# Optimization experiments

Measured on AMD Instinct MI355X. Metric: run time of the kernel, lower is better.

The kernel has to match this reference:

```python
import jax, jax.numpy as jnp
import numpy as np

LAYER_NUM = 2
HEAD_NUM = 2
LN_EPS = 1e-3  # Keras LayerNormalization default epsilon


def setup_inputs() -> dict:
    key = jax.random.key(0)
    ks = jax.random.split(key, 8)
    B, F, E = 16384, 40, 64
    s = 1.0 / np.sqrt(E)
    return {
        "x": jax.random.normal(ks[0], (B, F, E), jnp.float32),
        "Wq": jax.random.normal(ks[1], (E, E), jnp.float32) * s,
        "bq": jnp.zeros((E,), jnp.float32),
        "Wk": jax.random.normal(ks[2], (E, E), jnp.float32) * s,
        "bk": jnp.zeros((E,), jnp.float32),
        "Wv": jax.random.normal(ks[3], (E, E), jnp.float32) * s,
        "bv": jnp.zeros((E,), jnp.float32),
        "Wr": jax.random.normal(ks[4], (E, E), jnp.float32) * s,
        "br": jnp.zeros((E,), jnp.float32),
        "gamma": jnp.ones((E,), jnp.float32),
        "beta": jnp.zeros((E,), jnp.float32),
    }


def _split_heads(t, H):
    # [B, F, E] -> [B, H, F, E//H]; equivalent to tf split(axis=2)+concat(axis=0)
    B, F, E = t.shape
    return t.reshape(B, F, H, E // H).transpose(0, 2, 1, 3)


def _merge_heads(t):
    # [B, H, F, Dh] -> [B, F, E]
    B, H, F, Dh = t.shape
    return t.transpose(0, 2, 1, 3).reshape(B, F, H * Dh)


def reference(x, Wq, bq, Wk, bk, Wv, bv, Wr, br, gamma, beta):
    H = HEAD_NUM
    out = x
    for _ in range(LAYER_NUM):  # same (shared) weights every iteration, as in Keras build()
        q = jax.nn.relu(out @ Wq + bq)
        k = jax.nn.relu(out @ Wk + bk)
        v = jax.nn.relu(out @ Wv + bv)
        res = jax.nn.relu(out @ Wr + br)
        qh = _split_heads(q, H)  # [B,H,F,Dh]
        kh = _split_heads(k, H)
        vh = _split_heads(v, H)
        Dh = qh.shape[-1]
        w = jnp.einsum("bhfd,bhgd->bhfg", qh, kh) / jnp.sqrt(jnp.float32(Dh))
        w = jax.nn.softmax(w, axis=-1)
        # dropout_rate=0.0 -> no dropout branch in the original module
        o = jnp.einsum("bhfg,bhgd->bhfd", w, vh)
        out = _merge_heads(o) + res
        out = jax.nn.relu(out)
        mu = jnp.mean(out, axis=-1, keepdims=True)
        var = jnp.mean(jnp.square(out - mu), axis=-1, keepdims=True)
        out = (out - mu) * jax.lax.rsqrt(var + LN_EPS) * gamma + beta
    return out
```

## Files before the change

kernel.cpp:

```cpp
#include <hip/hip_runtime.h>
#include <math.h>

#define TF 40
#define FP 48
#define TE 64
#define RS 72
#define NTH 256
#define CURSZ (FP * RS)

typedef __attribute__((ext_vector_type(8))) short bf16x8;
typedef __attribute__((ext_vector_type(4))) float f32x4;
typedef unsigned int uint;
typedef unsigned short ushort;

#define MFMA(a, b, c) __builtin_amdgcn_mfma_f32_16x16x32_bf16(a, b, c, 0, 0, 0)

__device__ __forceinline__ ushort f2bf(float x) {
    union { float f; uint u; } a; a.f = x;
    uint r = a.u + 0x7FFFu + ((a.u >> 16) & 1u);
    return (ushort)(r >> 16);
}
__device__ __forceinline__ float bf2f(ushort h) {
    union { uint u; float f; } a; a.u = ((uint)h) << 16;
    return a.f;
}

__global__ void prep_wfrags(const float* __restrict__ Wq, const float* __restrict__ Wk,
                            const float* __restrict__ Wv, const float* __restrict__ Wr,
                            ushort* __restrict__ wsf) {
    int idx = blockIdx.x * blockDim.x + threadIdx.x;
    int j    = idx & 7;
    int lane = (idx >> 3) & 63;
    int et   = (idx >> 9) & 3;
    int k2   = (idx >> 11) & 1;
    int mat  = (idx >> 12) & 3;
    const float* W = (mat == 0) ? Wq : (mat == 1) ? Wk : (mat == 2) ? Wv : Wr;
    int k = k2 * 32 + (lane >> 4) * 8 + j;
    int e = et * 16 + (lane & 15);
    wsf[idx] = f2bf(W[k * TE + e]);
}

__global__ __launch_bounds__(NTH)
void autoint_mfma(const float* __restrict__ x,
                  const float* __restrict__ bq, const float* __restrict__ bk,
                  const float* __restrict__ bv, const float* __restrict__ br,
                  const float* __restrict__ gamma, const float* __restrict__ beta,
                  const ushort* __restrict__ wsf,
                  float* __restrict__ out) {
    __shared__ ushort sCur[2][CURSZ];
    __shared__ ushort sQ[CURSZ];
    __shared__ ushort sK[CURSZ];
    __shared__ ushort sVT[TE * RS];
    __shared__ float  sRed[2][4][FP];

    const int t  = threadIdx.x;
    const int w  = t >> 6;
    const int l  = t & 63;
    const int r0 = l & 15;
    const int kg = l >> 4;
    const int ec = 16 * w + r0;
    const size_t base = (size_t)blockIdx.x * (TF * TE);

    const float bQ = bq[ec], bK = bk[ec], bV = bv[ec], bR = br[ec];
    const float gV = gamma[ec], btV = beta[ec];

    const bf16x8* wsv = (const bf16x8*)wsf;
    const bf16x8 wq0 = wsv[((0*2+0)*4 + w)*64 + l], wq1 = wsv[((0*2+1)*4 + w)*64 + l];
    const bf16x8 wk0 = wsv[((1*2+0)*4 + w)*64 + l], wk1 = wsv[((1*2+1)*4 + w)*64 + l];
    const bf16x8 wv0 = wsv[((2*2+0)*4 + w)*64 + l], wv1 = wsv[((2*2+1)*4 + w)*64 + l];
    const bf16x8 wr0 = wsv[((3*2+0)*4 + w)*64 + l], wr1 = wsv[((3*2+1)*4 + w)*64 + l];

    {
        const float4* xb4 = (const float4*)(x + base);
        for (int i = t; i < TF * TE / 4; i += NTH) {
            float4 xv = xb4[i];
            int f = i >> 4, c = (i & 15) << 2;
            ushort h0 = f2bf(xv.x), h1 = f2bf(xv.y), h2 = f2bf(xv.z), h3 = f2bf(xv.w);
            uint2 ph; ph.x = h0 | ((uint)h1 << 16); ph.y = h2 | ((uint)h3 << 16);
            *(uint2*)&sCur[0][f * RS + c] = ph;
            ushort l0 = f2bf(xv.x - bf2f(h0)), l1 = f2bf(xv.y - bf2f(h1));
            ushort l2 = f2bf(xv.z - bf2f(h2)), l3 = f2bf(xv.w - bf2f(h3));
            uint2 pl; pl.x = l0 | ((uint)l1 << 16); pl.y = l2 | ((uint)l3 << 16);
            *(uint2*)&sCur[1][f * RS + c] = pl;
        }
        for (int i = t; i < 576; i += NTH) {
            int part = i / 288, rem = i - part * 288;
            int row = 40 + rem / 36, c = rem % 36;
            ((uint*)&sCur[part][0])[row * 36 + c] = 0u;
        }
        for (int i = t; i < 768; i += NTH) {
            int row = i / 12, c = i % 12;
            ((uint*)&sVT[0])[row * 36 + 24 + c] = 0u;
        }
    }
    __syncthreads();

    for (int lay = 0; lay < 2; ++lay) {
        f32x4 res0, res1, res2;
        #pragma unroll
        for (int ft = 0; ft < 3; ++ft) {
            const int rowb = (ft * 16 + r0) * RS + kg * 8;
            bf16x8 ah0 = *(const bf16x8*)&sCur[0][rowb];
            bf16x8 ah1 = *(const bf16x8*)&sCur[0][rowb + 32];
            bf16x8 al0 = *(const bf16x8*)&sCur[1][rowb];
            bf16x8 al1 = *(const bf16x8*)&sCur[1][rowb + 32];
            f32x4 z = {0.f, 0.f, 0.f, 0.f};
            f32x4 aq = z, ak = z, av = z, ar = z;
            aq = MFMA(ah0, wq0, aq); aq = MFMA(ah1, wq1, aq);
            aq = MFMA(al0, wq0, aq); aq = MFMA(al1, wq1, aq);
            ak = MFMA(ah0, wk0, ak); ak = MFMA(ah1, wk1, ak);
            ak = MFMA(al0, wk0, ak); ak = MFMA(al1, wk1, ak);
            av = MFMA(ah0, wv0, av); av = MFMA(ah1, wv1, av);
            av = MFMA(al0, wv0, av); av = MFMA(al1, wv1, av);
            ar = MFMA(ah0, wr0, ar); ar = MFMA(ah1, wr1, ar);
            ar = MFMA(al0, wr0, ar); ar = MFMA(al1, wr1, ar);
            ushort pv[4];
            f32x4 rr;
            #pragma unroll
            for (int r = 0; r < 4; ++r) {
                const int fr = ft * 16 + 4 * kg + r;
                sQ[fr * RS + ec] = f2bf(fmaxf(aq[r] + bQ, 0.f));
                sK[fr * RS + ec] = f2bf(fmaxf(ak[r] + bK, 0.f));
                pv[r] = f2bf(fmaxf(av[r] + bV, 0.f));
                rr[r] = fmaxf(ar[r] + bR, 0.f);
            }
            uint2 pk; pk.x = pv[0] | ((uint)pv[1] << 16); pk.y = pv[2] | ((uint)pv[3] << 16);
            *(uint2*)&sVT[ec * RS + ft * 16 + 4 * kg] = pk;
            if (ft == 0) res0 = rr; else if (ft == 1) res1 = rr; else res2 = rr;
        }
        __syncthreads();

        for (int i = t; i < 768; i += NTH) {
            int ph = i / 384, rem = i - ph * 384;
            int row = rem >> 3, c = rem & 7;
            ((uint*)&sCur[ph][0])[row * 36 + 24 + c] = 0u;
        }

        auto p2unit = [&](int u) {
            const int h  = (u >= 3) ? 1 : 0;
            const int ft = u - 3 * h;
            const int co = 32 * h + kg * 8;
            bf16x8 a  = *(const bf16x8*)&sQ[(ft * 16 + r0) * RS + co];
            bf16x8 b0 = *(const bf16x8*)&sK[(r0) * RS + co];
            bf16x8 b1 = *(const bf16x8*)&sK[(16 + r0) * RS + co];
            bf16x8 b2 = *(const bf16x8*)&sK[(32 + r0) * RS + co];
            f32x4 z = {0.f, 0.f, 0.f, 0.f};
            f32x4 c0 = MFMA(a, b0, z);
            f32x4 c1 = MFMA(a, b1, z);
            f32x4 c2 = MFMA(a, b2, z);
            ushort* Ph = &sCur[h][0];
            #pragma unroll
            for (int r = 0; r < 4; ++r) {
                const float SC = 0.17677669529663687f;
                float v0 = c0[r] * SC, v1 = c1[r] * SC;
                float v2 = (r0 < 8) ? c2[r] * SC : -3.0e38f;
                float m = fmaxf(fmaxf(v0, v1), v2);
                m = fmaxf(m, __shfl_xor(m, 1)); m = fmaxf(m, __shfl_xor(m, 2));
                m = fmaxf(m, __shfl_xor(m, 4)); m = fmaxf(m, __shfl_xor(m, 8));
                float p0 = exp2f((v0 - m) * 1.44269504f);
                float p1 = exp2f((v1 - m) * 1.44269504f);
                float p2 = (r0 < 8) ? exp2f((v2 - m) * 1.44269504f) : 0.f;
                float s = p0 + p1 + p2;
                s += __shfl_xor(s, 1); s += __shfl_xor(s, 2);
                s += __shfl_xor(s, 4); s += __shfl_xor(s, 8);
                float inv = 1.0f / s;
                const int fr = ft * 16 + 4 * kg + r;
                Ph[fr * RS +      r0] = f2bf(p0 * inv);
                Ph[fr * RS + 16 + r0] = f2bf(p1 * inv);
                Ph[fr * RS + 32 + r0] = f2bf(p2 * inv);
            }
        };
        p2unit(w);
        if (w < 2) p2unit(w + 4);
        __syncthreads();

        const int h = w >> 1;
        const ushort* Ph = &sCur[h][0];
        bf16x8 vb0 = *(const bf16x8*)&sVT[ec * RS + kg * 8];
        bf16x8 vb1 = *(const bf16x8*)&sVT[ec * RS + 32 + kg * 8];
        float vo0[4], vo1[4], vo2[4];
        #pragma unroll
        for (int ft = 0; ft < 3; ++ft) {
            bf16x8 pa0 = *(const bf16x8*)&Ph[(ft * 16 + r0) * RS + kg * 8];
            bf16x8 pa1 = *(const bf16x8*)&Ph[(ft * 16 + r0) * RS + 32 + kg * 8];
            f32x4 o = (ft == 0) ? res0 : (ft == 1) ? res1 : res2;
            o = MFMA(pa0, vb0, o);
            o = MFMA(pa1, vb1, o);
            #pragma unroll
            for (int r = 0; r < 4; ++r) {
                float v = fmaxf(o[r], 0.f);
                if (ft == 0) vo0[r] = v; else if (ft == 1) vo1[r] = v; else vo2[r] = v;
            }
        }

        #pragma unroll
        for (int ft = 0; ft < 3; ++ft) {
            #pragma unroll
            for (int r = 0; r < 4; ++r) {
                float v = (ft == 0) ? vo0[r] : (ft == 1) ? vo1[r] : vo2[r];
                float a = v, b = v * v;
                a += __shfl_xor(a, 1); b += __shfl_xor(b, 1);
                a += __shfl_xor(a, 2); b += __shfl_xor(b, 2);
                a += __shfl_xor(a, 4); b += __shfl_xor(b, 4);
                a += __shfl_xor(a, 8); b += __shfl_xor(b, 8);
                if (r0 == 0) {
                    const int fr = ft * 16 + 4 * kg + r;
                    sRed[0][w][fr] = a;
                    sRed[1][w][fr] = b;
                }
            }
        }
        __syncthreads();

        #pragma unroll
        for (int ft = 0; ft < 3; ++ft) {
            #pragma unroll
            for (int r = 0; r < 4; ++r) {
                const int fr = ft * 16 + 4 * kg + r;
                float v  = (ft == 0) ? vo0[r] : (ft == 1) ? vo1[r] : vo2[r];
                float s1 = sRed[0][0][fr] + sRed[0][1][fr] + sRed[0][2][fr] + sRed[0][3][fr];
                float s2 = sRed[1][0][fr] + sRed[1][1][fr] + sRed[1][2][fr] + sRed[1][3][fr];
                float mu  = s1 * 0.015625f;
                float var = fmaf(s2, 0.015625f, -mu * mu);
                float yv  = (v - mu) * rsqrtf(var + 1e-3f) * gV + btV;
                if (fr < TF) {
                    if (lay == 0) {
                        ushort hh = f2bf(yv);
                        sCur[0][fr * RS + ec] = hh;
                        sCur[1][fr * RS + ec] = f2bf(yv - bf2f(hh));
                    } else {
                        out[base + fr * TE + ec] = yv;
                    }
                }
            }
        }
        __syncthreads();
    }
}

extern "C" void kernel_launch(void* const* d_in, const int* in_sizes, int n_in,
                              void* d_out, int out_size, void* d_ws, size_t ws_size,
                              hipStream_t stream) {
    const float* x     = (const float*)d_in[0];
    const float* Wq    = (const float*)d_in[1];
    const float* bq    = (const float*)d_in[2];
    const float* Wk    = (const float*)d_in[3];
    const float* bk    = (const float*)d_in[4];
    const float* Wv    = (const float*)d_in[5];
    const float* bv    = (const float*)d_in[6];
    const float* Wr    = (const float*)d_in[7];
    const float* br    = (const float*)d_in[8];
    const float* gamma = (const float*)d_in[9];
    const float* beta  = (const float*)d_in[10];
    float* outp = (float*)d_out;
    ushort* wsf = (ushort*)d_ws;

    prep_wfrags<<<64, 256, 0, stream>>>(Wq, Wk, Wv, Wr, wsf);

    const int B = in_sizes[0] / (TF * TE);
    autoint_mfma<<<B, NTH, 0, stream>>>(x, bq, bk, bv, br, gamma, beta, wsf, outp);
}
```

Baseline: 826.7 us.

## Drop split-bf16 input precision, pack LDS pool, use hardware bf16 convert

Removes the hi/lo bf16 split of activations, which halves the projection MFMAs and the shared-memory traffic for the current tile. Packs all shared buffers into one smaller pool with narrower strides for P and V^T, uses v_cvt_pk_bf16_f32 and the raw exp2 builtin, and skips padded rows in stores and reductions. It also drops the last barrier. The aim is lower LDS use and less ALU/MFMA work, at the cost of accuracy from single-bf16 rounding of the inputs.

```diff
diff --git a/kernel.cpp b/kernel.cpp
--- a/kernel.cpp
+++ b/kernel.cpp
@@ -1,12 +1,17 @@
 #include <hip/hip_runtime.h>
-#include <math.h>
 
 #define TF 40
-#define FP 48
 #define TE 64
-#define RS 72
 #define NTH 256
-#define CURSZ (FP * RS)
+
+#define RSC 72
+#define RSP 48
+#define OFF_CUR 0
+#define OFF_P1  3456
+#define OFF_Q   5760
+#define OFF_K   8640
+#define OFF_VT  11520
+#define POOLSZ  14592
 
 typedef __attribute__((ext_vector_type(8))) short bf16x8;
 typedef __attribute__((ext_vector_type(4))) float f32x4;
@@ -15,14 +20,13 @@
 
 #define MFMA(a, b, c) __builtin_amdgcn_mfma_f32_16x16x32_bf16(a, b, c, 0, 0, 0)
 
+__device__ __forceinline__ uint cvtpk(float a, float b) {
+    uint r; asm("v_cvt_pk_bf16_f32 %0, %1, %2" : "=v"(r) : "v"(a), "v"(b)); return r;
+}
 __device__ __forceinline__ ushort f2bf(float x) {
     union { float f; uint u; } a; a.f = x;
     uint r = a.u + 0x7FFFu + ((a.u >> 16) & 1u);
     return (ushort)(r >> 16);
-}
-__device__ __forceinline__ float bf2f(ushort h) {
-    union { uint u; float f; } a; a.u = ((uint)h) << 16;
-    return a.f;
 }
 
 __global__ void prep_wfrags(const float* __restrict__ Wq, const float* __restrict__ Wk,
@@ -35,9 +39,7 @@
     int k2   = (idx >> 11) & 1;
     int mat  = (idx >> 12) & 3;
     const float* W = (mat == 0) ? Wq : (mat == 1) ? Wk : (mat == 2) ? Wv : Wr;
-    int k = k2 * 32 + (lane >> 4) * 8 + j;
-    int e = et * 16 + (lane & 15);
-    wsf[idx] = f2bf(W[k * TE + e]);
+    wsf[idx] = f2bf(W[(k2 * 32 + (lane >> 4) * 8 + j) * TE + et * 16 + (lane & 15)]);
 }
 
 __global__ __launch_bounds__(NTH)
@@ -47,11 +49,8 @@
                   const float* __restrict__ gamma, const float* __restrict__ beta,
                   const ushort* __restrict__ wsf,
                   float* __restrict__ out) {
-    __shared__ ushort sCur[2][CURSZ];
-    __shared__ ushort sQ[CURSZ];
-    __shared__ ushort sK[CURSZ];
-    __shared__ ushort sVT[TE * RS];
-    __shared__ float  sRed[2][4][FP];
+    __shared__ ushort pool[POOLSZ];
+    __shared__ float  sRed[4][TF][2];
 
     const int t  = threadIdx.x;
     const int w  = t >> 6;
@@ -65,33 +64,20 @@
     const float gV = gamma[ec], btV = beta[ec];
 
     const bf16x8* wsv = (const bf16x8*)wsf;
-    const bf16x8 wq0 = wsv[((0*2+0)*4 + w)*64 + l], wq1 = wsv[((0*2+1)*4 + w)*64 + l];
-    const bf16x8 wk0 = wsv[((1*2+0)*4 + w)*64 + l], wk1 = wsv[((1*2+1)*4 + w)*64 + l];
-    const bf16x8 wv0 = wsv[((2*2+0)*4 + w)*64 + l], wv1 = wsv[((2*2+1)*4 + w)*64 + l];
-    const bf16x8 wr0 = wsv[((3*2+0)*4 + w)*64 + l], wr1 = wsv[((3*2+1)*4 + w)*64 + l];
+    const bf16x8 wq0 = wsv[(0*4 + w)*64 + l], wq1 = wsv[(1*4 + w)*64 + l];
+    const bf16x8 wk0 = wsv[(2*4 + w)*64 + l], wk1 = wsv[(3*4 + w)*64 + l];
+    const bf16x8 wv0 = wsv[(4*4 + w)*64 + l], wv1 = wsv[(5*4 + w)*64 + l];
+    const bf16x8 wr0 = wsv[(6*4 + w)*64 + l], wr1 = wsv[(7*4 + w)*64 + l];
 
     {
         const float4* xb4 = (const float4*)(x + base);
         for (int i = t; i < TF * TE / 4; i += NTH) {
             float4 xv = xb4[i];
             int f = i >> 4, c = (i & 15) << 2;
-            ushort h0 = f2bf(xv.x), h1 = f2bf(xv.y), h2 = f2bf(xv.z), h3 = f2bf(xv.w);
-            uint2 ph; ph.x = h0 | ((uint)h1 << 16); ph.y = h2 | ((uint)h3 << 16);
-            *(uint2*)&sCur[0][f * RS + c] = ph;
-            ushort l0 = f2bf(xv.x - bf2f(h0)), l1 = f2bf(xv.y - bf2f(h1));
-            ushort l2 = f2bf(xv.z - bf2f(h2)), l3 = f2bf(xv.w - bf2f(h3));
-            uint2 pl; pl.x = l0 | ((uint)l1 << 16); pl.y = l2 | ((uint)l3 << 16);
-            *(uint2*)&sCur[1][f * RS + c] = pl;
-        }
-        for (int i = t; i < 576; i += NTH) {
-            int part = i / 288, rem = i - part * 288;
-            int row = 40 + rem / 36, c = rem % 36;
-            ((uint*)&sCur[part][0])[row * 36 + c] = 0u;
-        }
-        for (int i = t; i < 768; i += NTH) {
-            int row = i / 12, c = i % 12;
-            ((uint*)&sVT[0])[row * 36 + 24 + c] = 0u;
-        }
+            uint2 ph; ph.x = cvtpk(xv.x, xv.y); ph.y = cvtpk(xv.z, xv.w);
+            *(uint2*)&pool[OFF_CUR + f * RSC + c] = ph;
+        }
+        for (int i = t; i < 288; i += NTH) ((uint*)pool)[1440 + i] = 0u;
     }
     __syncthreads();
 
@@ -99,56 +85,53 @@
         f32x4 res0, res1, res2;
         #pragma unroll
         for (int ft = 0; ft < 3; ++ft) {
-            const int rowb = (ft * 16 + r0) * RS + kg * 8;
-            bf16x8 ah0 = *(const bf16x8*)&sCur[0][rowb];
-            bf16x8 ah1 = *(const bf16x8*)&sCur[0][rowb + 32];
-            bf16x8 al0 = *(const bf16x8*)&sCur[1][rowb];
-            bf16x8 al1 = *(const bf16x8*)&sCur[1][rowb + 32];
+            const int rowb = (ft * 16 + r0) * RSC + kg * 8;
+            bf16x8 a0 = *(const bf16x8*)&pool[OFF_CUR + rowb];
+            bf16x8 a1 = *(const bf16x8*)&pool[OFF_CUR + rowb + 32];
             f32x4 z = {0.f, 0.f, 0.f, 0.f};
             f32x4 aq = z, ak = z, av = z, ar = z;
-            aq = MFMA(ah0, wq0, aq); aq = MFMA(ah1, wq1, aq);
-            aq = MFMA(al0, wq0, aq); aq = MFMA(al1, wq1, aq);
-            ak = MFMA(ah0, wk0, ak); ak = MFMA(ah1, wk1, ak);
-            ak = MFMA(al0, wk0, ak); ak = MFMA(al1, wk1, ak);
-            av = MFMA(ah0, wv0, av); av = MFMA(ah1, wv1, av);
-            av = MFMA(al0, wv0, av); av = MFMA(al1, wv1, av);
-            ar = MFMA(ah0, wr0, ar); ar = MFMA(ah1, wr1, ar);
-            ar = MFMA(al0, wr0, ar); ar = MFMA(al1, wr1, ar);
-            ushort pv[4];
-            f32x4 rr;
-            #pragma unroll
-            for (int r = 0; r < 4; ++r) {
-                const int fr = ft * 16 + 4 * kg + r;
-                sQ[fr * RS + ec] = f2bf(fmaxf(aq[r] + bQ, 0.f));
-                sK[fr * RS + ec] = f2bf(fmaxf(ak[r] + bK, 0.f));
-                pv[r] = f2bf(fmaxf(av[r] + bV, 0.f));
-                rr[r] = fmaxf(ar[r] + bR, 0.f);
-            }
-            uint2 pk; pk.x = pv[0] | ((uint)pv[1] << 16); pk.y = pv[2] | ((uint)pv[3] << 16);
-            *(uint2*)&sVT[ec * RS + ft * 16 + 4 * kg] = pk;
+            aq = MFMA(a0, wq0, aq); aq = MFMA(a1, wq1, aq);
+            ak = MFMA(a0, wk0, ak); ak = MFMA(a1, wk1, ak);
+            av = MFMA(a0, wv0, av); av = MFMA(a1, wv1, av);
+            ar = MFMA(a0, wr0, ar); ar = MFMA(a1, wr1, ar);
+            const int fb = ft * 16 + 4 * kg;
+            if (fb < TF) {
+                uint q01 = cvtpk(fmaxf(aq[0]+bQ,0.f), fmaxf(aq[1]+bQ,0.f));
+                uint q23 = cvtpk(fmaxf(aq[2]+bQ,0.f), fmaxf(aq[3]+bQ,0.f));
+                pool[OFF_Q + (fb+0)*RSC + ec] = (ushort)q01;
+                pool[OFF_Q + (fb+1)*RSC + ec] = (ushort)(q01 >> 16);
+                pool[OFF_Q + (fb+2)*RSC + ec] = (ushort)q23;
+                pool[OFF_Q + (fb+3)*RSC + ec] = (ushort)(q23 >> 16);
+                uint k01 = cvtpk(fmaxf(ak[0]+bK,0.f), fmaxf(ak[1]+bK,0.f));
+                uint k23 = cvtpk(fmaxf(ak[2]+bK,0.f), fmaxf(ak[3]+bK,0.f));
+                pool[OFF_K + (fb+0)*RSC + ec] = (ushort)k01;
+                pool[OFF_K + (fb+1)*RSC + ec] = (ushort)(k01 >> 16);
+                pool[OFF_K + (fb+2)*RSC + ec] = (ushort)k23;
+                pool[OFF_K + (fb+3)*RSC + ec] = (ushort)(k23 >> 16);
+            }
+            uint2 pv;
+            pv.x = cvtpk(fmaxf(av[0]+bV,0.f), fmaxf(av[1]+bV,0.f));
+            pv.y = cvtpk(fmaxf(av[2]+bV,0.f), fmaxf(av[3]+bV,0.f));
+            *(uint2*)&pool[OFF_VT + ec * RSP + fb] = pv;
+            f32x4 rr = {fmaxf(ar[0]+bR,0.f), fmaxf(ar[1]+bR,0.f),
+                        fmaxf(ar[2]+bR,0.f), fmaxf(ar[3]+bR,0.f)};
             if (ft == 0) res0 = rr; else if (ft == 1) res1 = rr; else res2 = rr;
         }
         __syncthreads();
-
-        for (int i = t; i < 768; i += NTH) {
-            int ph = i / 384, rem = i - ph * 384;
-            int row = rem >> 3, c = rem & 7;
-            ((uint*)&sCur[ph][0])[row * 36 + 24 + c] = 0u;
-        }
 
         auto p2unit = [&](int u) {
             const int h  = (u >= 3) ? 1 : 0;
             const int ft = u - 3 * h;
             const int co = 32 * h + kg * 8;
-            bf16x8 a  = *(const bf16x8*)&sQ[(ft * 16 + r0) * RS + co];
-            bf16x8 b0 = *(const bf16x8*)&sK[(r0) * RS + co];
-            bf16x8 b1 = *(const bf16x8*)&sK[(16 + r0) * RS + co];
-            bf16x8 b2 = *(const bf16x8*)&sK[(32 + r0) * RS + co];
+            bf16x8 a  = *(const bf16x8*)&pool[OFF_Q + (ft * 16 + r0) * RSC + co];
+            bf16x8 b0 = *(const bf16x8*)&pool[OFF_K + (r0) * RSC + co];
+            bf16x8 b1 = *(const bf16x8*)&pool[OFF_K + (16 + r0) * RSC + co];
+            bf16x8 b2 = *(const bf16x8*)&pool[OFF_K + (32 + r0) * RSC + co];
             f32x4 z = {0.f, 0.f, 0.f, 0.f};
             f32x4 c0 = MFMA(a, b0, z);
             f32x4 c1 = MFMA(a, b1, z);
             f32x4 c2 = MFMA(a, b2, z);
-            ushort* Ph = &sCur[h][0];
+            ushort* Ph = pool + (h ? OFF_P1 : OFF_CUR);
             #pragma unroll
             for (int r = 0; r < 4; ++r) {
                 const float SC = 0.17677669529663687f;
@@ -157,32 +140,38 @@
                 float m = fmaxf(fmaxf(v0, v1), v2);
                 m = fmaxf(m, __shfl_xor(m, 1)); m = fmaxf(m, __shfl_xor(m, 2));
                 m = fmaxf(m, __shfl_xor(m, 4)); m = fmaxf(m, __shfl_xor(m, 8));
-                float p0 = exp2f((v0 - m) * 1.44269504f);
-                float p1 = exp2f((v1 - m) * 1.44269504f);
-                float p2 = (r0 < 8) ? exp2f((v2 - m) * 1.44269504f) : 0.f;
-                float s = p0 + p1 + p2;
+                const float LOG2E = 1.44269504f;
+                float p0 = __builtin_amdgcn_exp2f((v0 - m) * LOG2E);
+                float p1 = __builtin_amdgcn_exp2f((v1 - m) * LOG2E);
+                float p2v = (r0 < 8) ? __builtin_amdgcn_exp2f((v2 - m) * LOG2E) : 0.f;
+                float s = p0 + p1 + p2v;
                 s += __shfl_xor(s, 1); s += __shfl_xor(s, 2);
                 s += __shfl_xor(s, 4); s += __shfl_xor(s, 8);
                 float inv = 1.0f / s;
                 const int fr = ft * 16 + 4 * kg + r;
-                Ph[fr * RS +      r0] = f2bf(p0 * inv);
-                Ph[fr * RS + 16 + r0] = f2bf(p1 * inv);
-                Ph[fr * RS + 32 + r0] = f2bf(p2 * inv);
+                uint p01 = cvtpk(p0 * inv, p1 * inv);
+                uint p22 = cvtpk(p2v * inv, p2v * inv);
+                Ph[fr * RSP +      r0] = (ushort)p01;
+                Ph[fr * RSP + 16 + r0] = (ushort)(p01 >> 16);
+                Ph[fr * RSP + 32 + r0] = (ushort)p22;
             }
         };
         p2unit(w);
         if (w < 2) p2unit(w + 4);
         __syncthreads();
 
-        const int h = w >> 1;
-        const ushort* Ph = &sCur[h][0];
-        bf16x8 vb0 = *(const bf16x8*)&sVT[ec * RS + kg * 8];
-        bf16x8 vb1 = *(const bf16x8*)&sVT[ec * RS + 32 + kg * 8];
+        const int hh = w >> 1;
+        const ushort* Ph = pool + (hh ? OFF_P1 : OFF_CUR);
+        const bf16x8 zz = {0,0,0,0,0,0,0,0};
+        bf16x8 vb0 = *(const bf16x8*)&pool[OFF_VT + ec * RSP + kg * 8];
+        bf16x8 vb1 = zz;
+        if (kg < 2) vb1 = *(const bf16x8*)&pool[OFF_VT + ec * RSP + 32 + kg * 8];
         float vo0[4], vo1[4], vo2[4];
         #pragma unroll
         for (int ft = 0; ft < 3; ++ft) {
-            bf16x8 pa0 = *(const bf16x8*)&Ph[(ft * 16 + r0) * RS + kg * 8];
-            bf16x8 pa1 = *(const bf16x8*)&Ph[(ft * 16 + r0) * RS + 32 + kg * 8];
+            bf16x8 pa0 = *(const bf16x8*)&Ph[(ft * 16 + r0) * RSP + kg * 8];
+            bf16x8 pa1 = zz;
+            if (kg < 2) pa1 = *(const bf16x8*)&Ph[(ft * 16 + r0) * RSP + 32 + kg * 8];
             f32x4 o = (ft == 0) ? res0 : (ft == 1) ? res1 : res2;
             o = MFMA(pa0, vb0, o);
             o = MFMA(pa1, vb1, o);
@@ -195,18 +184,17 @@
 
         #pragma unroll
         for (int ft = 0; ft < 3; ++ft) {
-            #pragma unroll
-            for (int r = 0; r < 4; ++r) {
-                float v = (ft == 0) ? vo0[r] : (ft == 1) ? vo1[r] : vo2[r];
-                float a = v, b = v * v;
-                a += __shfl_xor(a, 1); b += __shfl_xor(b, 1);
-                a += __shfl_xor(a, 2); b += __shfl_xor(b, 2);
-                a += __shfl_xor(a, 4); b += __shfl_xor(b, 4);
-                a += __shfl_xor(a, 8); b += __shfl_xor(b, 8);
-                if (r0 == 0) {
-                    const int fr = ft * 16 + 4 * kg + r;
-                    sRed[0][w][fr] = a;
-                    sRed[1][w][fr] = b;
+            const int fb = ft * 16 + 4 * kg;
+            if (fb < TF) {
+                #pragma unroll
+                for (int r = 0; r < 4; ++r) {
+                    float v = (ft == 0) ? vo0[r] : (ft == 1) ? vo1[r] : vo2[r];
+                    float a = v, b = v * v;
+                    a += __shfl_xor(a, 1); b += __shfl_xor(b, 1);
+                    a += __shfl_xor(a, 2); b += __shfl_xor(b, 2);
+                    a += __shfl_xor(a, 4); b += __shfl_xor(b, 4);
+                    a += __shfl_xor(a, 8); b += __shfl_xor(b, 8);
+                    if (r0 == 0) *(float2*)&sRed[w][fb + r][0] = make_float2(a, b);
                 }
             }
         }
@@ -214,27 +202,37 @@
 
         #pragma unroll
         for (int ft = 0; ft < 3; ++ft) {
-            #pragma unroll
-            for (int r = 0; r < 4; ++r) {
-                const int fr = ft * 16 + 4 * kg + r;
-                float v  = (ft == 0) ? vo0[r] : (ft == 1) ? vo1[r] : vo2[r];
-                float s1 = sRed[0][0][fr] + sRed[0][1][fr] + sRed[0][2][fr] + sRed[0][3][fr];
-                float s2 = sRed[1][0][fr] + sRed[1][1][fr] + sRed[1][2][fr] + sRed[1][3][fr];
-                float mu  = s1 * 0.015625f;
-                float var = fmaf(s2, 0.015625f, -mu * mu);
-                float yv  = (v - mu) * rsqrtf(var + 1e-3f) * gV + btV;
-                if (fr < TF) {
-                    if (lay == 0) {
-                        ushort hh = f2bf(yv);
-                        sCur[0][fr * RS + ec] = hh;
-                        sCur[1][fr * RS + ec] = f2bf(yv - bf2f(hh));
-                    } else {
-                        out[base + fr * TE + ec] = yv;
+            const int fb = ft * 16 + 4 * kg;
+            if (fb < TF) {
+                float y[4];
+                #pragma unroll
+                for (int r = 0; r < 4; ++r) {
+                    const int fr = fb + r;
+                    float s1 = 0.f, s2 = 0.f;
+                    #pragma unroll
+                    for (int ww = 0; ww < 4; ++ww) {
+                        float2 p = *(const float2*)&sRed[ww][fr][0];
+                        s1 += p.x; s2 += p.y;
                     }
+                    float v   = (ft == 0) ? vo0[r] : (ft == 1) ? vo1[r] : vo2[r];
+                    float mu  = s1 * 0.015625f;
+                    float var = fmaf(s2, 0.015625f, -mu * mu);
+                    y[r] = (v - mu) * rsqrtf(var + 1e-3f) * gV + btV;
                 }
-            }
-        }
-        __syncthreads();
+                if (lay == 0) {
+                    uint c01 = cvtpk(y[0], y[1]), c23 = cvtpk(y[2], y[3]);
+                    pool[OFF_CUR + (fb + 0) * RSC + ec] = (ushort)c01;
+                    pool[OFF_CUR + (fb + 1) * RSC + ec] = (ushort)(c01 >> 16);
+                    pool[OFF_CUR + (fb + 2) * RSC + ec] = (ushort)c23;
+                    pool[OFF_CUR + (fb + 3) * RSC + ec] = (ushort)(c23 >> 16);
+                } else {
+                    #pragma unroll
+                    for (int r = 0; r < 4; ++r)
+                        out[base + (fb + r) * TE + ec] = y[r];
+                }
+            }
+        }
+        if (lay == 0) __syncthreads();
     }
 }
 
```

Result: faster. 749.1 us (-9.4%).
